# Kernel optimization log

Measured on AMD Instinct MI355X. Metric: run time of the kernel, lower is better.

Reference implementation:

```python
import jax, jax.numpy as jnp
import numpy as np

B, S, H, NH, HD = 4, 2048, 2048, 16, 128
SCALE = HD ** -0.5


def rotate_half(x):
    x1, x2 = jnp.split(x, 2, axis=-1)
    return jnp.concatenate([-x2, x1], axis=-1)


def setup_inputs() -> dict:
    key = jax.random.key(0)
    ks = jax.random.split(key, 8)
    x = jax.random.normal(ks[0], (B, S, H), dtype=jnp.float32)
    # RoPE tables for positions 0..S-1, standard theta=10000 construction
    inv_freq = 1.0 / (10000.0 ** (jnp.arange(0, HD, 2, dtype=jnp.float32) / HD))
    t = jnp.arange(S, dtype=jnp.float32)
    freqs = jnp.einsum('s,d->sd', t, inv_freq)          # [S, HD/2]
    emb = jnp.concatenate([freqs, freqs], axis=-1)      # [S, HD]
    cos, sin = jnp.cos(emb), jnp.sin(emb)
    # causal mask: True = masked (future positions)
    mask = jnp.triu(jnp.ones((S, S), dtype=bool), k=1)
    std = H ** -0.5
    Wq = jax.random.normal(ks[1], (H, H), dtype=jnp.float32) * std
    Wk = jax.random.normal(ks[2], (H, H), dtype=jnp.float32) * std
    Wv = jax.random.normal(ks[3], (H, H), dtype=jnp.float32) * std
    Wo = jax.random.normal(ks[4], (H, H), dtype=jnp.float32) * std
    return {"x": x, "cos": cos, "sin": sin, "mask": mask,
            "Wq": Wq, "Wk": Wk, "Wv": Wv, "Wo": Wo}


def reference(x, cos, sin, mask, Wq, Wk, Wv, Wo):
    # projections: nn.Linear(bias=False) => x @ W.T
    def proj(W):
        y = jnp.einsum('bsh,ih->bsi', x, W)             # [B,S,inner]
        return y.reshape(B, S, NH, HD).transpose(0, 2, 1, 3)  # [B,NH,S,HD]
    q, k, v = proj(Wq), proj(Wk), proj(Wv)
    # RoPE (rotate-half), cos/sin broadcast over batch & heads
    c = cos[None, None, :, :]
    s = sin[None, None, :, :]
    q = q * c + rotate_half(q) * s
    k = k * c + rotate_half(k) * s
    # attention
    attn = jnp.einsum('bhqd,bhkd->bhqk', q, k) * SCALE
    attn = jnp.where(mask[None, None, :, :], -jnp.inf, attn)
    attn = jax.nn.softmax(attn, axis=-1)
    out = jnp.einsum('bhqk,bhkd->bhqd', attn, v)
    out = out.transpose(0, 2, 1, 3).reshape(B, S, NH * HD)
    y = jnp.einsum('bsi,hi->bsh', out, Wo)
    return y, k, v
```

## Files before the change

kernel.cpp:

```cpp
#include <hip/hip_runtime.h>
#include <hip/hip_bf16.h>
#include <math.h>

typedef __bf16 bf16_t;
typedef __bf16 bf16x8 __attribute__((ext_vector_type(8)));
typedef __bf16 bf16x4v __attribute__((ext_vector_type(4)));
typedef float  f32x4  __attribute__((ext_vector_type(4)));
typedef float  f32x16 __attribute__((ext_vector_type(16)));
typedef unsigned int u32x4 __attribute__((ext_vector_type(4)));

constexpr int CB = 4, CS = 2048, CH = 2048, CNH = 16, CHD = 128;
constexpr int CM = CB * CS;
constexpr float CSCALE = 0.08838834764831845f;
constexpr float CL2E   = 1.4426950408889634f;
constexpr float CSC2   = CSCALE * CL2E;

__device__ __forceinline__ float fexp2(float x) {
  float r;
  asm("v_exp_f32 %0, %1" : "=v"(r) : "v"(x));
  return r;
}

__device__ __forceinline__ void g2l16(const void* g, void* l) {
  __builtin_amdgcn_global_load_lds(
      (const __attribute__((address_space(1))) void*)g,
      (__attribute__((address_space(3))) void*)l, 16, 0, 0);
}

__global__ __launch_bounds__(256) void cvt_all(const float* __restrict__ x,
                                               const float* __restrict__ Wq,
                                               const float* __restrict__ Wk,
                                               const float* __restrict__ Wv,
                                               const float* __restrict__ Wo,
                                               bf16_t* __restrict__ xb,
                                               bf16_t* __restrict__ wqb,
                                               bf16_t* __restrict__ wkb,
                                               bf16_t* __restrict__ wvb,
                                               bf16_t* __restrict__ wob) {
  constexpr int NX = CM * CH / 4;
  constexpr int NW = CH * CH / 4;
  const int i = blockIdx.x * 256 + threadIdx.x;
  const float* src;
  bf16_t* dst;
  int off;
  if (i < NX) {
    src = x; dst = xb; off = i;
  } else {
    const int j = i - NX;
    const int sel = j / NW;
    off = j - sel * NW;
    src = (sel == 0) ? Wq : (sel == 1) ? Wk : (sel == 2) ? Wv : Wo;
    dst = (sel == 0) ? wqb : (sel == 1) ? wkb : (sel == 2) ? wvb : wob;
  }
  float4 v = reinterpret_cast<const float4*>(src)[off];
  bf16x4v o = {(bf16_t)v.x, (bf16_t)v.y, (bf16_t)v.z, (bf16_t)v.w};
  reinterpret_cast<bf16x4v*>(dst)[off] = o;
}

__device__ __forceinline__ void gemm256sq_core(const bf16_t* __restrict__ A,
                                               const bf16_t* __restrict__ Bm,
                                               bf16_t (*As2)[4][64 * 64],
                                               bf16_t (*Bs2)[4][64 * 64],
                                               int row0, int col0,
                                               f32x4 (&acc)[8][4]) {
  const int tid = threadIdx.x, lane = tid & 63, w = tid >> 6;
  const int wm = w >> 2, wn = w & 3;
  constexpr int NKT = CH / 64;
  const int id = w * 64 + lane;
  const int rl = id >> 3, ck = id & 7;

  auto stA = [&](int buf, int kt, int q) {
    const int row = q * 64 + rl;
    g2l16(A + (size_t)(row0 + row) * CH + kt * 64 + ((ck ^ (row & 7)) << 3),
          &As2[buf][q][id * 8]);
  };
  auto stB = [&](int buf, int kt, int q) {
    const int row = q * 64 + rl;
    g2l16(Bm + (size_t)(col0 + row) * CH + kt * 64 + ((ck ^ (row & 7)) << 3),
          &Bs2[buf][q][id * 8]);
  };
  auto rdA = [&](int buf, int r, int c) -> bf16x8 {
    return *(const bf16x8*)(&As2[buf][r >> 6][(r & 63) * 64 + ((c ^ (r & 7)) << 3)]);
  };
  auto rdB = [&](int buf, int r, int c) -> bf16x8 {
    return *(const bf16x8*)(&Bs2[buf][r >> 6][(r & 63) * 64 + ((c ^ (r & 7)) << 3)]);
  };

#pragma unroll
  for (int q = 0; q < 4; ++q) stB(0, 0, q);
#pragma unroll
  for (int q = 0; q < 4; ++q) stA(0, 0, q);
  asm volatile("s_waitcnt vmcnt(0)" ::: "memory");
  __builtin_amdgcn_s_barrier();
  __builtin_amdgcn_sched_barrier(0);

  const int ar0 = wm * 128 + (lane & 15);
  const int br0 = wn * 64 + (lane & 15);
  const int chi = lane >> 4;

  for (int t = 0; t < NKT; ++t) {
    const int buf = t & 1, nbuf = buf ^ 1;
    const bool pf = (t + 1 < NKT);
    bf16x8 bb[4][2], aa[2][2];

#pragma unroll
    for (int p = 0; p < 4; ++p) {
      if (p == 0) {
#pragma unroll
        for (int nf = 0; nf < 4; ++nf)
#pragma unroll
          for (int kk = 0; kk < 2; ++kk)
            bb[nf][kk] = rdB(buf, br0 + nf * 16, kk * 4 + chi);
      }
#pragma unroll
      for (int i = 0; i < 2; ++i)
#pragma unroll
        for (int kk = 0; kk < 2; ++kk)
          aa[i][kk] = rdA(buf, ar0 + (2 * p + i) * 16, kk * 4 + chi);

      if (pf) {
        if (p == 0) { stB(nbuf, t + 1, 0); stB(nbuf, t + 1, 1); }
        if (p == 1) { stA(nbuf, t + 1, 0); stA(nbuf, t + 1, 2); }
        if (p == 2) { stB(nbuf, t + 1, 2); stB(nbuf, t + 1, 3); }
        if (p == 3) { stA(nbuf, t + 1, 1); stA(nbuf, t + 1, 3); }
      }

      __builtin_amdgcn_s_barrier();
      asm volatile("s_waitcnt lgkmcnt(0)" ::: "memory");
      __builtin_amdgcn_sched_barrier(0);
      __builtin_amdgcn_s_setprio(1);
#pragma unroll
      for (int i = 0; i < 2; ++i)
#pragma unroll
        for (int nf = 0; nf < 4; ++nf)
#pragma unroll
          for (int kk = 0; kk < 2; ++kk)
            acc[2 * p + i][nf] = __builtin_amdgcn_mfma_f32_16x16x32_bf16(
                aa[i][kk], bb[nf][kk], acc[2 * p + i][nf], 0, 0, 0);
      __builtin_amdgcn_s_setprio(0);

      if (p == 1) {
        if (pf) { asm volatile("s_waitcnt vmcnt(4)" ::: "memory"); }
        else    { asm volatile("s_waitcnt vmcnt(0)" ::: "memory"); }
      }
      if (p == 3 && pf) { asm volatile("s_waitcnt vmcnt(2)" ::: "memory"); }
      __builtin_amdgcn_s_barrier();
      __builtin_amdgcn_sched_barrier(0);
    }
  }
}

__global__ __launch_bounds__(512, 1) void qkv_gemm(const bf16_t* __restrict__ xb,
                                                   const bf16_t* __restrict__ wqb,
                                                   const bf16_t* __restrict__ wkb,
                                                   const bf16_t* __restrict__ wvb,
                                                   const float* __restrict__ cosd,
                                                   const float* __restrict__ sind,
                                                   bf16_t* __restrict__ qraw,
                                                   bf16_t* __restrict__ knat,
                                                   bf16_t* __restrict__ vt2,
                                                   float* __restrict__ kout,
                                                   float* __restrict__ vout) {
  __shared__ __align__(16) bf16_t LSD[2][2][4][64 * 64];
  const int z = blockIdx.z;
  const bf16_t* Bm = (z == 0) ? wqb : ((z == 1) ? wkb : wvb);
  const int row0 = blockIdx.x * 256, col0 = blockIdx.y * 256;
  f32x4 acc[8][4] = {};
  gemm256sq_core(xb, Bm, LSD[0], LSD[1], row0, col0, acc);

  const int tid = threadIdx.x, lane = tid & 63, w = tid >> 6;
  const int wm = w >> 2, wn = w & 3;

  bf16_t* L = &LSD[0][0][0][0];
#pragma unroll
  for (int i = 0; i < 8; ++i)
#pragma unroll
    for (int j = 0; j < 4; ++j) {
      const int col = wn * 64 + j * 16 + (lane & 15);
#pragma unroll
      for (int r = 0; r < 4; ++r) {
        const int row = wm * 128 + i * 16 + (lane >> 4) * 4 + r;
        L[row * 256 + (((col >> 3) ^ (row & 31)) << 3) + (col & 7)] =
            (bf16_t)acc[i][j][r];
      }
    }
  if (z == 2) {
#pragma unroll
    for (int i = 0; i < 8; ++i)
#pragma unroll
      for (int j = 0; j < 4; ++j) {
        const int gr0 = row0 + wm * 128 + i * 16 + (lane >> 4) * 4;
        const int gc = col0 + wn * 64 + j * 16 + (lane & 15);
        const int b = gr0 >> 11, s0 = gr0 & (CS - 1);
        const int nh = gc >> 7, hd = gc & (CHD - 1);
        const int bh = b * CNH + nh;
        bf16x4v pv = {(bf16_t)acc[i][j][0], (bf16_t)acc[i][j][1],
                      (bf16_t)acc[i][j][2], (bf16_t)acc[i][j][3]};
        *(bf16x4v*)(vt2 + (((size_t)bh * (CS / 16) + (s0 >> 4)) * CHD + hd) * 16 +
                    (s0 & 15)) = pv;
      }
  }
  __syncthreads();

  if (z == 0) {
#pragma unroll
    for (int k = 0; k < 16; ++k) {
      const int u = k * 512 + tid;
      const int row = u >> 5, ch = u & 31;
      bf16x8 v = *(const bf16x8*)&L[row * 256 + ((ch ^ (row & 31)) << 3)];
      const int gr = row0 + row, gc = col0 + ch * 8;
      const int b = gr >> 11, s = gr & (CS - 1), nh = gc >> 7, hd = gc & (CHD - 1);
      *(bf16x8*)&qraw[((size_t)(b * CNH + nh) * CS + s) * CHD + hd] = v;
    }
  } else if (z == 2) {
#pragma unroll
    for (int k = 0; k < 16; ++k) {
      const int u = k * 512 + tid;
      const int row = u >> 5, ch = u & 31;
      bf16x8 v = *(const bf16x8*)&L[row * 256 + ((ch ^ (row & 31)) << 3)];
      const int gr = row0 + row, gc = col0 + ch * 8;
      const int b = gr >> 11, s = gr & (CS - 1), nh = gc >> 7, hd = gc & (CHD - 1);
      float o[8];
#pragma unroll
      for (int e = 0; e < 8; ++e) o[e] = (float)v[e];
      float* vp = vout + ((size_t)(b * CNH + nh) * CS + s) * CHD + hd;
      *(float4*)(vp)     = *(float4*)(o);
      *(float4*)(vp + 4) = *(float4*)(o + 4);
    }
  } else {
#pragma unroll
    for (int k = 0; k < 16; ++k) {
      const int u = k * 512 + tid;
      const int row = u >> 5, ch = u & 31;
      bf16x8 v = *(const bf16x8*)&L[row * 256 + ((ch ^ (row & 31)) << 3)];
      bf16x8 p = *(const bf16x8*)&L[row * 256 + (((ch ^ 8) ^ (row & 31)) << 3)];
      const int gr = row0 + row, gc = col0 + ch * 8;
      const int b = gr >> 11, s = gr & (CS - 1), nh = gc >> 7, hd = gc & (CHD - 1);
      const float sgn = (hd < 64) ? -1.f : 1.f;
      float c[8], sn[8], o[8];
      *(float4*)(c)      = *(const float4*)(cosd + (size_t)s * CHD + hd);
      *(float4*)(c + 4)  = *(const float4*)(cosd + (size_t)s * CHD + hd + 4);
      *(float4*)(sn)     = *(const float4*)(sind + (size_t)s * CHD + hd);
      *(float4*)(sn + 4) = *(const float4*)(sind + (size_t)s * CHD + hd + 4);
#pragma unroll
      for (int e = 0; e < 8; ++e)
        o[e] = (float)v[e] * c[e] + sgn * (float)p[e] * sn[e];
      float* kp = kout + ((size_t)(b * CNH + nh) * CS + s) * CHD + hd;
      *(float4*)(kp)     = *(float4*)(o);
      *(float4*)(kp + 4) = *(float4*)(o + 4);
    }
#pragma unroll
    for (int k = 0; k < 16; ++k) {
      const int u = k * 512 + tid;
      const int s = u & 255, cc = u >> 8;
      bf16x8 v = *(const bf16x8*)&L[s * 256 + ((cc ^ (s & 31)) << 3)];
      bf16x8 p = *(const bf16x8*)&L[s * 256 + (((cc ^ 8) ^ (s & 31)) << 3)];
      const int gr = row0 + s, gc = col0 + cc * 8;
      const int b = gr >> 11, sg = gr & (CS - 1), nh = gc >> 7, hd = gc & (CHD - 1);
      const float sgn = (hd < 64) ? -1.f : 1.f;
      float c[8], sn[8];
      *(float4*)(c)      = *(const float4*)(cosd + (size_t)sg * CHD + hd);
      *(float4*)(c + 4)  = *(const float4*)(cosd + (size_t)sg * CHD + hd + 4);
      *(float4*)(sn)     = *(const float4*)(sind + (size_t)sg * CHD + hd);
      *(float4*)(sn + 4) = *(const float4*)(sind + (size_t)sg * CHD + hd + 4);
      bf16x8 o;
#pragma unroll
      for (int e = 0; e < 8; ++e)
        o[e] = (bf16_t)((float)v[e] * c[e] + sgn * (float)p[e] * sn[e]);
      const int pan = hd >> 4, half = (hd >> 3) & 1;
      *(bf16x8*)&knat[(((size_t)(b * CNH + nh) * 8 + pan) * CS + sg) * 16 +
                      half * 8] = o;
    }
  }
}

__global__ __launch_bounds__(512, 1) void y_gemm(const bf16_t* __restrict__ ob,
                                                 const bf16_t* __restrict__ wob,
                                                 float* __restrict__ yout) {
  __shared__ __align__(16) bf16_t LSD[2][2][4][64 * 64];
  const int row0 = blockIdx.x * 256, col0 = blockIdx.y * 256;
  f32x4 acc[8][4] = {};
  gemm256sq_core(ob, wob, LSD[0], LSD[1], row0, col0, acc);
  const int tid = threadIdx.x, lane = tid & 63, w = tid >> 6;
  const int wm = w >> 2, wn = w & 3;
  float* Lf = (float*)&LSD[0][0][0][0];

#pragma unroll
  for (int half = 0; half < 2; ++half) {
    if (wm == half) {
#pragma unroll
      for (int i = 0; i < 8; ++i)
#pragma unroll
        for (int j = 0; j < 4; ++j) {
          const int col = wn * 64 + j * 16 + (lane & 15);
#pragma unroll
          for (int r = 0; r < 4; ++r) {
            const int rl = i * 16 + (lane >> 4) * 4 + r;
            Lf[rl * 256 + col] = acc[i][j][r];
          }
        }
    }
    __syncthreads();
#pragma unroll
    for (int k = 0; k < 16; ++k) {
      const int u = k * 512 + tid;
      const int rl = u >> 6, ch = u & 63;
      float4 v = *(const float4*)&Lf[rl * 256 + ch * 4];
      const int gr = row0 + half * 128 + rl, gc = col0 + ch * 4;
      *(float4*)&yout[(size_t)gr * CH + gc] = v;
    }
    __syncthreads();
  }
}

__global__ __launch_bounds__(128) void attn_kernel(const bf16_t* __restrict__ qb,
                                                   const bf16_t* __restrict__ kn,
                                                   const bf16_t* __restrict__ v2,
                                                   const float* __restrict__ cosd,
                                                   const float* __restrict__ sind,
                                                   bf16_t* __restrict__ ob) {
  __shared__ float Os[32][129];
  __shared__ float Ms[32], Ls[32];
  const int tid = threadIdx.x, lane = tid & 63, wh = tid >> 6;
  const int hi = lane >> 5, l31 = lane & 31;

  const int swz = (blockIdx.x & 7) * 512 + (blockIdx.x >> 3);
  const int bh = swz >> 6;
  const int qt = 63 - (swz & 63);

  const int b = bh >> 4, nh = bh & (CNH - 1);
  const bf16_t* kbase = kn + (size_t)bh * 8 * CS * 16;
  const bf16_t* vbase = v2 + (size_t)bh * (CS / 16) * CHD * 16;
  const int qw0 = qt * 32;
  const int qrow = qw0 + l31;

  bf16x8 bq[8];
  {
    const bf16_t* qp = qb + ((size_t)bh * CS + qrow) * CHD + hi * 8;
    bf16x8 raw[8];
#pragma unroll
    for (int ks = 0; ks < 8; ++ks) raw[ks] = *(const bf16x8*)(qp + ks * 16);
#pragma unroll
    for (int p = 0; p < 4; ++p) {
      const int d0 = p * 16 + hi * 8;
      float cc[8], ss[8];
      *(float4*)(cc)     = *(const float4*)(cosd + (size_t)qrow * CHD + d0);
      *(float4*)(cc + 4) = *(const float4*)(cosd + (size_t)qrow * CHD + d0 + 4);
      *(float4*)(ss)     = *(const float4*)(sind + (size_t)qrow * CHD + d0);
      *(float4*)(ss + 4) = *(const float4*)(sind + (size_t)qrow * CHD + d0 + 4);
#pragma unroll
      for (int e = 0; e < 8; ++e) {
        const float x1 = (float)raw[p][e], x2 = (float)raw[p + 4][e];
        bq[p][e]     = (bf16_t)(x1 * cc[e] - x2 * ss[e]);
        bq[p + 4][e] = (bf16_t)(x2 * cc[e] + x1 * ss[e]);
      }
    }
  }

  float m_ = -INFINITY, l_ = 0.f;
  f32x16 o_[4] = {};

  const int nt = (qt >> 1) + 1;
  for (int kt = wh; kt < nt; kt += 2) {
    const int kvb = kt * 64;

    bf16x8 ak[2][8];
#pragma unroll
    for (int kb2 = 0; kb2 < 2; ++kb2) {
      const bf16_t* kr = kbase + (size_t)(kvb + kb2 * 32 + l31) * 16 + hi * 8;
#pragma unroll
      for (int ks = 0; ks < 8; ++ks)
        ak[kb2][ks] = *(const bf16x8*)(kr + (size_t)ks * CS * 16);
    }

    f32x16 st[2] = {};
#pragma unroll
    for (int kb2 = 0; kb2 < 2; ++kb2)
#pragma unroll
      for (int ks = 0; ks < 8; ++ks)
        st[kb2] = __builtin_amdgcn_mfma_f32_32x32x16_bf16(ak[kb2][ks], bq[ks],
                                                          st[kb2], 0, 0, 0);

    bf16x8 av[4][4];
#pragma unroll
    for (int hb = 0; hb < 4; ++hb) {
      const bf16_t* vr = vbase + ((size_t)(kvb >> 4) * CHD + hb * 32 + l31) * 16 + hi * 8;
#pragma unroll
      for (int ks = 0; ks < 4; ++ks)
        av[hb][ks] = *(const bf16x8*)(vr + (size_t)ks * CHD * 16);
    }

    const bool anymask = (kvb + 63) > qw0;
#pragma unroll
    for (int blk = 0; blk < 2; ++blk)
#pragma unroll
      for (int r = 0; r < 16; ++r) {
        float xv = st[blk][r] * CSC2;
        if (anymask) {
          const int kv = kvb + blk * 32 + 4 * hi + (r & 3) + 8 * (r >> 2);
          if (kv > qrow) xv = -INFINITY;
        }
        st[blk][r] = xv;
      }

    float tmax = st[0][0];
#pragma unroll
    for (int r = 1; r < 16; ++r) tmax = fmaxf(tmax, st[0][r]);
#pragma unroll
    for (int r = 0; r < 16; ++r) tmax = fmaxf(tmax, st[1][r]);
    tmax = fmaxf(tmax, __shfl_xor(tmax, 32, 64));

    if (__any(tmax - m_ > 8.0f)) {
      const float mn = fmaxf(m_, tmax);
      const float corr = fexp2(m_ - mn);
      m_ = mn;
      l_ *= corr;
#pragma unroll
      for (int hb = 0; hb < 4; ++hb) o_[hb] *= corr;
    }

    float psum = 0.f;
#pragma unroll
    for (int blk = 0; blk < 2; ++blk)
#pragma unroll
      for (int r = 0; r < 16; ++r) {
        const float pv = fexp2(st[blk][r] - m_);
        st[blk][r] = pv;
        psum += pv;
      }
    psum += __shfl_xor(psum, 32, 64);
    l_ += psum;

    bf16x8 pb[4];
#pragma unroll
    for (int ks = 0; ks < 4; ++ks) {
      const int blk = ks >> 1, r0 = (ks & 1) * 8;
      unsigned pw0, pw1, pw2, pw3;
      asm("v_cvt_pk_bf16_f32 %0, %1, %2" : "=v"(pw0) : "v"(st[blk][r0 + 0]), "v"(st[blk][r0 + 1]));
      asm("v_cvt_pk_bf16_f32 %0, %1, %2" : "=v"(pw2) : "v"(st[blk][r0 + 4]), "v"(st[blk][r0 + 5]));
      asm("v_cvt_pk_bf16_f32 %0, %1, %2" : "=v"(pw1) : "v"(st[blk][r0 + 2]), "v"(st[blk][r0 + 3]));
      asm("v_cvt_pk_bf16_f32 %0, %1, %2" : "=v"(pw3) : "v"(st[blk][r0 + 6]), "v"(st[blk][r0 + 7]));
      asm("v_permlane32_swap_b32 %0, %1" : "+v"(pw0), "+v"(pw2));
      asm("v_permlane32_swap_b32 %0, %1" : "+v"(pw1), "+v"(pw3));
      u32x4 pk = {pw0, pw1, pw2, pw3};
      pb[ks] = *reinterpret_cast<bf16x8*>(&pk);
    }

#pragma unroll
    for (int hb = 0; hb < 4; ++hb)
#pragma unroll
      for (int ks = 0; ks < 4; ++ks)
        o_[hb] = __builtin_amdgcn_mfma_f32_32x32x16_bf16(av[hb][ks], pb[ks],
                                                         o_[hb], 0, 0, 0);
  }

  if (wh == 1) {
#pragma unroll
    for (int hb = 0; hb < 4; ++hb)
#pragma unroll
      for (int r = 0; r < 16; ++r) {
        const int hd = 32 * hb + 4 * hi + (r & 3) + 8 * (r >> 2);
        Os[l31][hd] = o_[hb][r];
      }
    if (hi == 0) { Ms[l31] = m_; Ls[l31] = l_; }
  }
  __builtin_amdgcn_s_barrier();
  if (wh == 1) return;

  const float m1 = Ms[l31], l1 = Ls[l31];
  const float mn = fmaxf(m_, m1);
  const float c0 = fexp2(m_ - mn), c1 = fexp2(m1 - mn);
  const float linv = 1.0f / (l_ * c0 + l1 * c1);
  bf16_t* orow = ob + ((size_t)(b * CS + qrow)) * CH + nh * CHD;
#pragma unroll
  for (int hb = 0; hb < 4; ++hb)
#pragma unroll
    for (int g = 0; g < 4; ++g) {
      const int hd0 = 32 * hb + 4 * hi + 8 * g;
      bf16x4v pv = {
          (bf16_t)((o_[hb][4 * g + 0] * c0 + Os[l31][hd0 + 0] * c1) * linv),
          (bf16_t)((o_[hb][4 * g + 1] * c0 + Os[l31][hd0 + 1] * c1) * linv),
          (bf16_t)((o_[hb][4 * g + 2] * c0 + Os[l31][hd0 + 2] * c1) * linv),
          (bf16_t)((o_[hb][4 * g + 3] * c0 + Os[l31][hd0 + 3] * c1) * linv)};
      *(bf16x4v*)(orow + hd0) = pv;
    }
}

extern "C" void kernel_launch(void* const* d_in, const int* in_sizes, int n_in,
                              void* d_out, int out_size, void* d_ws, size_t ws_size,
                              hipStream_t stream) {
  const float* x    = (const float*)d_in[0];
  const float* cosd = (const float*)d_in[1];
  const float* sind = (const float*)d_in[2];
  const float* Wq = (const float*)d_in[4];
  const float* Wk = (const float*)d_in[5];
  const float* Wv = (const float*)d_in[6];
  const float* Wo = (const float*)d_in[7];

  float* yout = (float*)d_out;
  float* kout = yout + (size_t)CM * CH;
  float* vout = kout + (size_t)CM * CH;

  char* ws = (char*)d_ws;
  size_t off = 0;
  auto wsalloc = [&](size_t bytes) {
    void* p = ws + off;
    off += (bytes + 255) & ~(size_t)255;
    return p;
  };
  bf16_t* xb   = (bf16_t*)wsalloc((size_t)CM * CH * 2);
  bf16_t* wqb  = (bf16_t*)wsalloc((size_t)CH * CH * 2);
  bf16_t* wkb  = (bf16_t*)wsalloc((size_t)CH * CH * 2);
  bf16_t* wvb  = (bf16_t*)wsalloc((size_t)CH * CH * 2);
  bf16_t* wob  = (bf16_t*)wsalloc((size_t)CH * CH * 2);
  bf16_t* qraw = (bf16_t*)wsalloc((size_t)CM * CH * 2);
  bf16_t* knat = (bf16_t*)wsalloc((size_t)CM * CH * 2);
  bf16_t* vt2  = (bf16_t*)wsalloc((size_t)CM * CH * 2);
  bf16_t* ob   = (bf16_t*)wsalloc((size_t)CM * CH * 2);

  cvt_all<<<(CM * CH / 4 + 4 * CH * CH / 4) / 256, 256, 0, stream>>>(
      x, Wq, Wk, Wv, Wo, xb, wqb, wkb, wvb, wob);

  qkv_gemm<<<dim3(CM / 256, CH / 256, 3), 512, 0, stream>>>(
      xb, wqb, wkb, wvb, cosd, sind, qraw, knat, vt2, kout, vout);
  attn_kernel<<<CB * CNH * (CS / 32), 128, 0, stream>>>(qraw, knat, vt2, cosd,
                                                        sind, ob);
  y_gemm<<<dim3(CM / 256, CH / 256), 512, 0, stream>>>(ob, wob, yout);
}
```

Before: 505.6 us.

## Share K/V tiles in LDS across four query warps with double-buffered async loads

The attention kernel now gives each block 128 query rows (four waves of 32) instead of 32 rows split across two waves over the KV range. K and V tiles are staged once per block into swizzled, double-buffered LDS with global_load_lds, so all four waves reuse them. This is meant to cut redundant global/L2 traffic for K and V and overlap the next tile's load with compute. Each wave now walks the full KV range itself, so the cross-wave softmax merge is gone. The cost is barrier synchronisation every tile, idle waves on causally dead tiles, and fewer, larger blocks.

After: 554.7 us. 9.7% more time.

```diff
diff --git a/kernel.cpp b/kernel.cpp
--- a/kernel.cpp
+++ b/kernel.cpp
@@ -313,25 +313,25 @@
   }
 }
 
-__global__ __launch_bounds__(128) void attn_kernel(const bf16_t* __restrict__ qb,
+__global__ __launch_bounds__(256) void attn_kernel(const bf16_t* __restrict__ qb,
                                                    const bf16_t* __restrict__ kn,
                                                    const bf16_t* __restrict__ v2,
                                                    const float* __restrict__ cosd,
                                                    const float* __restrict__ sind,
                                                    bf16_t* __restrict__ ob) {
-  __shared__ float Os[32][129];
-  __shared__ float Ms[32], Ls[32];
-  const int tid = threadIdx.x, lane = tid & 63, wh = tid >> 6;
+  __shared__ __align__(16) bf16_t Ks[2][64 * 128];
+  __shared__ __align__(16) bf16_t Vs[2][128 * 64];
+  const int tid = threadIdx.x, lane = tid & 63, w = tid >> 6;
   const int hi = lane >> 5, l31 = lane & 31;
 
-  const int swz = (blockIdx.x & 7) * 512 + (blockIdx.x >> 3);
-  const int bh = swz >> 6;
-  const int qt = 63 - (swz & 63);
+  const int swz = (blockIdx.x & 7) * 128 + (blockIdx.x >> 3);
+  const int bh = swz >> 4;
+  const int qt = 15 - (swz & 15);
 
   const int b = bh >> 4, nh = bh & (CNH - 1);
   const bf16_t* kbase = kn + (size_t)bh * 8 * CS * 16;
   const bf16_t* vbase = v2 + (size_t)bh * (CS / 16) * CHD * 16;
-  const int qw0 = qt * 32;
+  const int qw0 = qt * 128 + w * 32;
   const int qrow = qw0 + l31;
 
   bf16x8 bq[8];
@@ -360,129 +360,152 @@
   float m_ = -INFINITY, l_ = 0.f;
   f32x16 o_[4] = {};
 
-  const int nt = (qt >> 1) + 1;
-  for (int kt = wh; kt < nt; kt += 2) {
+  auto stage = [&](int buf, int kt) {
     const int kvb = kt * 64;
-
-    bf16x8 ak[2][8];
-#pragma unroll
-    for (int kb2 = 0; kb2 < 2; ++kb2) {
-      const bf16_t* kr = kbase + (size_t)(kvb + kb2 * 32 + l31) * 16 + hi * 8;
-#pragma unroll
-      for (int ks = 0; ks < 8; ++ks)
-        ak[kb2][ks] = *(const bf16x8*)(kr + (size_t)ks * CS * 16);
-    }
-
-    f32x16 st[2] = {};
-#pragma unroll
-    for (int kb2 = 0; kb2 < 2; ++kb2)
-#pragma unroll
-      for (int ks = 0; ks < 8; ++ks)
-        st[kb2] = __builtin_amdgcn_mfma_f32_32x32x16_bf16(ak[kb2][ks], bq[ks],
-                                                          st[kb2], 0, 0, 0);
-
-    bf16x8 av[4][4];
-#pragma unroll
-    for (int hb = 0; hb < 4; ++hb) {
-      const bf16_t* vr = vbase + ((size_t)(kvb >> 4) * CHD + hb * 32 + l31) * 16 + hi * 8;
-#pragma unroll
-      for (int ks = 0; ks < 4; ++ks)
-        av[hb][ks] = *(const bf16x8*)(vr + (size_t)ks * CHD * 16);
-    }
-
-    const bool anymask = (kvb + 63) > qw0;
-#pragma unroll
-    for (int blk = 0; blk < 2; ++blk)
-#pragma unroll
-      for (int r = 0; r < 16; ++r) {
-        float xv = st[blk][r] * CSC2;
-        if (anymask) {
-          const int kv = kvb + blk * 32 + 4 * hi + (r & 3) + 8 * (r >> 2);
-          if (kv > qrow) xv = -INFINITY;
+#pragma unroll
+    for (int i = 0; i < 4; ++i) {
+      const int c = i * 256 + tid;
+      const int r = c >> 4, ck = c & 15;
+      const int g = ck ^ (r & 15);
+      g2l16(kbase + (size_t)(g >> 1) * CS * 16 + (size_t)(kvb + r) * 16 + (g & 1) * 8,
+            &Ks[buf][(size_t)(i * 256 + (tid & ~63)) * 8 + (size_t)lane * 8]);
+    }
+#pragma unroll
+    for (int i = 0; i < 4; ++i) {
+      const int c = i * 256 + tid;
+      const int r = c >> 3, ck = c & 7;
+      const int g = ck ^ (r & 7);
+      g2l16(vbase + (size_t)((kvb >> 4) + (g >> 1)) * CHD * 16 + (size_t)r * 16 +
+                (g & 1) * 8,
+            &Vs[buf][(size_t)(i * 256 + (tid & ~63)) * 8 + (size_t)lane * 8]);
+    }
+  };
+
+  const int nt = 2 * qt + 2;
+  stage(0, 0);
+  int cur = 0;
+
+  for (int kt = 0; kt < nt; ++kt) {
+    if (kt + 1 < nt) {
+      stage(cur ^ 1, kt + 1);
+      asm volatile("s_waitcnt vmcnt(8)" ::: "memory");
+    } else {
+      asm volatile("s_waitcnt vmcnt(0)" ::: "memory");
+    }
+    __builtin_amdgcn_s_barrier();
+    __builtin_amdgcn_sched_barrier(0);
+
+    const int kvb = kt * 64;
+    const bool dead = kvb > qw0 + 31;
+    if (!dead) {
+      bf16x8 ak[2][8];
+#pragma unroll
+      for (int kb2 = 0; kb2 < 2; ++kb2) {
+        const int krow = kb2 * 32 + l31;
+#pragma unroll
+        for (int ks = 0; ks < 8; ++ks) {
+          const int ck = (ks * 2 + hi) ^ (krow & 15);
+          ak[kb2][ks] = *(const bf16x8*)&Ks[cur][krow * 128 + (ck << 3)];
         }
-        st[blk][r] = xv;
-      }
-
-    float tmax = st[0][0];
-#pragma unroll
-    for (int r = 1; r < 16; ++r) tmax = fmaxf(tmax, st[0][r]);
-#pragma unroll
-    for (int r = 0; r < 16; ++r) tmax = fmaxf(tmax, st[1][r]);
-    tmax = fmaxf(tmax, __shfl_xor(tmax, 32, 64));
-
-    if (__any(tmax - m_ > 8.0f)) {
-      const float mn = fmaxf(m_, tmax);
-      const float corr = fexp2(m_ - mn);
-      m_ = mn;
-      l_ *= corr;
-#pragma unroll
-      for (int hb = 0; hb < 4; ++hb) o_[hb] *= corr;
-    }
-
-    float psum = 0.f;
-#pragma unroll
-    for (int blk = 0; blk < 2; ++blk)
-#pragma unroll
-      for (int r = 0; r < 16; ++r) {
-        const float pv = fexp2(st[blk][r] - m_);
-        st[blk][r] = pv;
-        psum += pv;
-      }
-    psum += __shfl_xor(psum, 32, 64);
-    l_ += psum;
-
-    bf16x8 pb[4];
-#pragma unroll
-    for (int ks = 0; ks < 4; ++ks) {
-      const int blk = ks >> 1, r0 = (ks & 1) * 8;
-      unsigned pw0, pw1, pw2, pw3;
-      asm("v_cvt_pk_bf16_f32 %0, %1, %2" : "=v"(pw0) : "v"(st[blk][r0 + 0]), "v"(st[blk][r0 + 1]));
-      asm("v_cvt_pk_bf16_f32 %0, %1, %2" : "=v"(pw2) : "v"(st[blk][r0 + 4]), "v"(st[blk][r0 + 5]));
-      asm("v_cvt_pk_bf16_f32 %0, %1, %2" : "=v"(pw1) : "v"(st[blk][r0 + 2]), "v"(st[blk][r0 + 3]));
-      asm("v_cvt_pk_bf16_f32 %0, %1, %2" : "=v"(pw3) : "v"(st[blk][r0 + 6]), "v"(st[blk][r0 + 7]));
-      asm("v_permlane32_swap_b32 %0, %1" : "+v"(pw0), "+v"(pw2));
-      asm("v_permlane32_swap_b32 %0, %1" : "+v"(pw1), "+v"(pw3));
-      u32x4 pk = {pw0, pw1, pw2, pw3};
-      pb[ks] = *reinterpret_cast<bf16x8*>(&pk);
-    }
-
-#pragma unroll
-    for (int hb = 0; hb < 4; ++hb)
-#pragma unroll
-      for (int ks = 0; ks < 4; ++ks)
-        o_[hb] = __builtin_amdgcn_mfma_f32_32x32x16_bf16(av[hb][ks], pb[ks],
-                                                         o_[hb], 0, 0, 0);
-  }
-
-  if (wh == 1) {
-#pragma unroll
-    for (int hb = 0; hb < 4; ++hb)
-#pragma unroll
-      for (int r = 0; r < 16; ++r) {
-        const int hd = 32 * hb + 4 * hi + (r & 3) + 8 * (r >> 2);
-        Os[l31][hd] = o_[hb][r];
-      }
-    if (hi == 0) { Ms[l31] = m_; Ls[l31] = l_; }
-  }
-  __builtin_amdgcn_s_barrier();
-  if (wh == 1) return;
-
-  const float m1 = Ms[l31], l1 = Ls[l31];
-  const float mn = fmaxf(m_, m1);
-  const float c0 = fexp2(m_ - mn), c1 = fexp2(m1 - mn);
-  const float linv = 1.0f / (l_ * c0 + l1 * c1);
+      }
+
+      f32x16 st[2] = {};
+#pragma unroll
+      for (int kb2 = 0; kb2 < 2; ++kb2)
+#pragma unroll
+        for (int ks = 0; ks < 8; ++ks)
+          st[kb2] = __builtin_amdgcn_mfma_f32_32x32x16_bf16(ak[kb2][ks], bq[ks],
+                                                            st[kb2], 0, 0, 0);
+
+      bf16x8 av[4][4];
+#pragma unroll
+      for (int hb = 0; hb < 4; ++hb) {
+        const int vrow = hb * 32 + l31;
+#pragma unroll
+        for (int ks = 0; ks < 4; ++ks) {
+          const int ck = (ks * 2 + hi) ^ (vrow & 7);
+          av[hb][ks] = *(const bf16x8*)&Vs[cur][vrow * 64 + (ck << 3)];
+        }
+      }
+
+      const bool anymask = (kvb + 63) > qw0;
+#pragma unroll
+      for (int blk = 0; blk < 2; ++blk)
+#pragma unroll
+        for (int r = 0; r < 16; ++r) {
+          float xv = st[blk][r] * CSC2;
+          if (anymask) {
+            const int kv = kvb + blk * 32 + 4 * hi + (r & 3) + 8 * (r >> 2);
+            if (kv > qrow) xv = -INFINITY;
+          }
+          st[blk][r] = xv;
+        }
+
+      float tmax = st[0][0];
+#pragma unroll
+      for (int r = 1; r < 16; ++r) tmax = fmaxf(tmax, st[0][r]);
+#pragma unroll
+      for (int r = 0; r < 16; ++r) tmax = fmaxf(tmax, st[1][r]);
+      tmax = fmaxf(tmax, __shfl_xor(tmax, 32, 64));
+
+      if (__any(tmax - m_ > 8.0f)) {
+        const float mn = fmaxf(m_, tmax);
+        const float corr = fexp2(m_ - mn);
+        m_ = mn;
+        l_ *= corr;
+#pragma unroll
+        for (int hb = 0; hb < 4; ++hb) o_[hb] *= corr;
+      }
+
+      float psum = 0.f;
+#pragma unroll
+      for (int blk = 0; blk < 2; ++blk)
+#pragma unroll
+        for (int r = 0; r < 16; ++r) {
+          const float pv = fexp2(st[blk][r] - m_);
+          st[blk][r] = pv;
+          psum += pv;
+        }
+      psum += __shfl_xor(psum, 32, 64);
+      l_ += psum;
+
+      bf16x8 pb[4];
+#pragma unroll
+      for (int ks = 0; ks < 4; ++ks) {
+        const int blk = ks >> 1, r0 = (ks & 1) * 8;
+        unsigned pw0, pw1, pw2, pw3;
+        asm("v_cvt_pk_bf16_f32 %0, %1, %2" : "=v"(pw0) : "v"(st[blk][r0 + 0]), "v"(st[blk][r0 + 1]));
+        asm("v_cvt_pk_bf16_f32 %0, %1, %2" : "=v"(pw2) : "v"(st[blk][r0 + 4]), "v"(st[blk][r0 + 5]));
+        asm("v_cvt_pk_bf16_f32 %0, %1, %2" : "=v"(pw1) : "v"(st[blk][r0 + 2]), "v"(st[blk][r0 + 3]));
+        asm("v_cvt_pk_bf16_f32 %0, %1, %2" : "=v"(pw3) : "v"(st[blk][r0 + 6]), "v"(st[blk][r0 + 7]));
+        asm("v_permlane32_swap_b32 %0, %1" : "+v"(pw0), "+v"(pw2));
+        asm("v_permlane32_swap_b32 %0, %1" : "+v"(pw1), "+v"(pw3));
+        u32x4 pk = {pw0, pw1, pw2, pw3};
+        pb[ks] = *reinterpret_cast<bf16x8*>(&pk);
+      }
+
+#pragma unroll
+      for (int hb = 0; hb < 4; ++hb)
+#pragma unroll
+        for (int ks = 0; ks < 4; ++ks)
+          o_[hb] = __builtin_amdgcn_mfma_f32_32x32x16_bf16(av[hb][ks], pb[ks],
+                                                           o_[hb], 0, 0, 0);
+    }
+
+    __builtin_amdgcn_s_barrier();
+    __builtin_amdgcn_sched_barrier(0);
+    cur ^= 1;
+  }
+
+  const float linv = 1.0f / l_;
   bf16_t* orow = ob + ((size_t)(b * CS + qrow)) * CH + nh * CHD;
 #pragma unroll
   for (int hb = 0; hb < 4; ++hb)
 #pragma unroll
     for (int g = 0; g < 4; ++g) {
-      const int hd0 = 32 * hb + 4 * hi + 8 * g;
-      bf16x4v pv = {
-          (bf16_t)((o_[hb][4 * g + 0] * c0 + Os[l31][hd0 + 0] * c1) * linv),
-          (bf16_t)((o_[hb][4 * g + 1] * c0 + Os[l31][hd0 + 1] * c1) * linv),
-          (bf16_t)((o_[hb][4 * g + 2] * c0 + Os[l31][hd0 + 2] * c1) * linv),
-          (bf16_t)((o_[hb][4 * g + 3] * c0 + Os[l31][hd0 + 3] * c1) * linv)};
-      *(bf16x4v*)(orow + hd0) = pv;
+      bf16x4v pv = {(bf16_t)(o_[hb][4 * g + 0] * linv), (bf16_t)(o_[hb][4 * g + 1] * linv),
+                    (bf16_t)(o_[hb][4 * g + 2] * linv), (bf16_t)(o_[hb][4 * g + 3] * linv)};
+      *(bf16x4v*)(orow + hb * 32 + 4 * hi + 8 * g) = pv;
     }
 }
 
@@ -523,7 +546,7 @@
 
   qkv_gemm<<<dim3(CM / 256, CH / 256, 3), 512, 0, stream>>>(
       xb, wqb, wkb, wvb, cosd, sind, qraw, knat, vt2, kout, vout);
-  attn_kernel<<<CB * CNH * (CS / 32), 128, 0, stream>>>(qraw, knat, vt2, cosd,
-                                                        sind, ob);
+  attn_kernel<<<CB * CNH * (CS / 128), 256, 0, stream>>>(qraw, knat, vt2, cosd,
+                                                         sind, ob);
   y_gemm<<<dim3(CM / 256, CH / 256), 512, 0, stream>>>(ob, wob, yout);
 }
```
